# Optimization experiments

Hardware: AMD Instinct MI355X
Metric: run time of the kernel (lower is better)

The kernel has to match this reference:

```python
import jax, jax.numpy as jnp
import numpy as np

B, T, C, H = 4, 1024, 2048, 16
HD = C // H          # head dim = 128 (even, as RoPE requires)
BLOCK = 1024         # config.block_size == config.max_block_size
NEG = -1e30          # finite stand-in for -inf in the additive attention bias


def setup_inputs() -> dict:
    key = jax.random.key(0)
    k1, k2, k3, k4, k5 = jax.random.split(key, 5)
    x = jax.random.normal(k1, (B, T, C), jnp.float32)
    cumulative_scores = jax.random.uniform(k2, (B, T), jnp.float32)  # kept small: fed to exp()
    token_index = jax.random.randint(k3, (B, T), 0, BLOCK, dtype=jnp.int32)
    padding_mask = jnp.ones((B, T), jnp.int32)
    # xavier-ish scale so softmax doesn't saturate
    W_attn = jax.random.normal(k4, (C, 3 * C), jnp.float32) / np.sqrt(C)
    W_proj = jax.random.normal(k5, (C, C), jnp.float32) / np.sqrt(C)
    return dict(x=x, cumulative_scores=cumulative_scores, token_index=token_index,
                padding_mask=padding_mask, W_attn=W_attn, W_proj=W_proj)


def _rotate_half(a):
    a1, a2 = a[..., : HD // 2], a[..., HD // 2:]
    return jnp.concatenate([-a2, a1], axis=-1)


def reference(x, cumulative_scores, token_index, padding_mask, W_attn, W_proj):
    # QKV projection (bias=False per config)
    qkv = x @ W_attn                                  # (B,T,3C)
    q, k, v = jnp.split(qkv, 3, axis=2)
    heads = lambda a: a.reshape(B, T, H, HD).transpose(0, 2, 1, 3)  # (B,H,T,HD)
    q, k, v = heads(q), heads(k), heads(v)

    # input-dependent partial rotation positions (exact replica of the original
    # scatter: token_index (B,T) fancy-indexes the last axis of a (B,BLOCK)
    # buffer, so counts are summed over ALL batch rows, as in the source)
    counts = jnp.zeros((B, BLOCK), jnp.float32).at[..., token_index].add(1.0)
    t = jnp.cumsum(jnp.take_along_axis(1.0 / (counts + 1e-10), token_index, axis=-1), axis=-1)  # (B,T)

    # RoPE with per-token positions t (seq_dim=-2, offset 0 for both q and k)
    inv_freq = 1.0 / (10000.0 ** (jnp.arange(0, HD, 2, dtype=jnp.float32) / HD))
    freqs = jnp.einsum('bt,j->btj', t, inv_freq)
    emb = jnp.concatenate([freqs, freqs], axis=-1)[:, None, :, :]   # (B,1,T,HD)
    sin, cos = jnp.sin(emb), jnp.cos(emb)
    q = q * cos + _rotate_half(q) * sin
    k = k * cos + _rotate_half(k) * sin

    # 'fork' plan overrides on the last rotary channel
    q = q.at[..., -1].set(1.0)
    k = k.at[..., -1].set(jnp.broadcast_to(cumulative_scores[:, None, :], (B, H, T)))

    # V rescaled by exp(cumulative_scores)
    v = v * jnp.exp(cumulative_scores)[:, None, :, None]

    # causal + key-padding additive bias, SDPA with scale 1/sqrt(HD)
    keep = jnp.tril(jnp.ones((T, T), bool))[None, None] & padding_mask.astype(bool)[:, None, None, :]
    scores = jnp.einsum('bhqd,bhkd->bhqk', q, k) / np.sqrt(HD)
    scores = jnp.where(keep, scores, NEG)
    attn = jax.nn.softmax(scores, axis=-1)
    y = jnp.einsum('bhqk,bhkd->bhqd', attn, v)

    y = y.transpose(0, 2, 1, 3).reshape(B, T, C)
    return y @ W_proj
```

## Files before the change

kernel.cpp:

```cpp
#include <hip/hip_runtime.h>

#define BB 4
#define TT 1024
#define CCH 2048
#define HH 16
#define HDIM 128
#define NBLK 1024
#define MM (BB*TT)
#define N1 (3*CCH)
#define NQT 16

typedef _Float16 f16;
typedef _Float16 half8 __attribute__((ext_vector_type(8)));
typedef _Float16 half4 __attribute__((ext_vector_type(4)));
typedef float floatx4 __attribute__((ext_vector_type(4)));

__device__ __forceinline__ void g2lds16(const void* g, void* l) {
    __builtin_amdgcn_global_load_lds((const __attribute__((address_space(1))) void*)g,
                                     (__attribute__((address_space(3))) void*)l, 16, 0, 0);
}

__global__ void k_prep(const float* __restrict__ Wa, const float* __restrict__ Wp,
                       const float* __restrict__ x,
                       f16* __restrict__ WaT, f16* __restrict__ WpT,
                       f16* __restrict__ x16) {
    int z = blockIdx.z;
    if (z == 2) {
        int i = (blockIdx.y * 192 + blockIdx.x) * 256 + threadIdx.x + threadIdx.y * 32;
        if (i >= MM * CCH / 4) return;
        float4 v = ((const float4*)x)[i];
        union { ushort4 u; f16 h[4]; } o;
        o.h[0] = (f16)v.x; o.h[1] = (f16)v.y; o.h[2] = (f16)v.z; o.h[3] = (f16)v.w;
        ((ushort4*)x16)[i] = o.u;
        return;
    }
    const float* in = (z == 0) ? Wa : Wp;
    f16* out = (z == 0) ? WaT : WpT;
    int Cc = (z == 0) ? N1 : CCH;
    if (blockIdx.x * 32 >= Cc) return;
    __shared__ float tile[32][33];
    int c0 = blockIdx.x * 32, r0 = blockIdx.y * 32;
    int tx = threadIdx.x, ty = threadIdx.y;
#pragma unroll
    for (int k = 0; k < 4; k++) {
        int r = ty + k * 8;
        tile[r][tx] = in[(size_t)(r0 + r) * Cc + c0 + tx];
    }
    __syncthreads();
#pragma unroll
    for (int k = 0; k < 4; k++) {
        int r = ty + k * 8;
        out[(size_t)(c0 + r) * CCH + r0 + tx] = (f16)tile[tx][r];
    }
}

__global__ void k_trv(const f16* __restrict__ in, f16* __restrict__ out) {
    __shared__ f16 tile[32][34];
    int bh = blockIdx.z;
    int h0 = blockIdx.x * 32, t0 = blockIdx.y * 32;
    int tx = threadIdx.x, ty = threadIdx.y;
#pragma unroll
    for (int k = 0; k < 4; k++) {
        int t = ty + k * 8;
        tile[t][tx] = in[((size_t)bh * TT + t0 + t) * HDIM + h0 + tx];
    }
    __syncthreads();
#pragma unroll
    for (int k = 0; k < 4; k++) {
        int r = ty + k * 8;
        out[((size_t)bh * HDIM + h0 + r) * TT + t0 + tx] = tile[tx][r];
    }
}

__global__ void k_hist(const int* __restrict__ tok, int* __restrict__ cnt) {
    int i = blockIdx.x * blockDim.x + threadIdx.x;
    if (i < MM) atomicAdd(cnt + tok[i], 1);
}

__global__ __launch_bounds__(1024) void k_scan(const int* __restrict__ tok,
                                               const int* __restrict__ cnt,
                                               const int* __restrict__ pm,
                                               float* __restrict__ tpos,
                                               float* __restrict__ pb) {
    __shared__ float s[TT];
    int b = blockIdx.x, t = threadIdx.x;
    s[t] = 1.0f / ((float)cnt[tok[b * TT + t]] + 1e-10f);
    __syncthreads();
    for (int off = 1; off < TT; off <<= 1) {
        float add = (t >= off) ? s[t - off] : 0.0f;
        __syncthreads();
        s[t] += add;
        __syncthreads();
    }
    tpos[b * TT + t] = s[t];
    pb[b * TT + t] = pm[b * TT + t] ? 0.0f : -1e30f;
}

__global__ void k_rope(const float* __restrict__ tpos, float2* __restrict__ tab) {
    int i = blockIdx.x * 256 + threadIdx.x;
    int row = i >> 6, j = i & 63;
    float f = tpos[row] * expf((float)j * -0.14391156929f);
    float sn, cn; sincosf(f, &sn, &cn);
    tab[i] = make_float2(cn, sn);
}

#define RA(buf, mf, ck) (*(const half8*)((const char*)As + ((buf) << 15) + aoffb + ((mf) << 11) + (ck)))
#define RB(buf, nf, ck) (*(const half8*)((const char*)Bs + ((buf) << 15) + boffb + ((nf) << 13) + (ck)))
#define STAGE(P, L, h, t) do { \
    g2lds16((P) + ((size_t)(h) << 18) + ((t) << 6) + src0, (L) + ((h) << 13) + (w << 9)); \
    g2lds16((P) + ((size_t)(h) << 18) + ((t) << 6) + src1, (L) + ((h) << 13) + ((8 + w) << 9)); \
} while (0)
#define MFMAQ(AF, BF, M0, N0) do { \
  _Pragma("unroll") for (int m_ = 0; m_ < 4; m_++) \
  _Pragma("unroll") for (int n_ = 0; n_ < 2; n_++) \
  _Pragma("unroll") for (int k_ = 0; k_ < 2; k_++) \
    acc[(M0) + m_][(N0) + n_] = __builtin_amdgcn_mfma_f32_16x16x32_f16(AF[m_][k_], BF[n_][k_], acc[(M0) + m_][(N0) + n_], 0, 0, 0); \
} while (0)
#define BAR() __builtin_amdgcn_s_barrier()
#define WLG0() asm volatile("s_waitcnt lgkmcnt(0)" ::: "memory")

template <int MODE>
__global__ __launch_bounds__(512, 2) void k_gemm8(const f16* __restrict__ A,
                                                  const f16* __restrict__ Bt,
                                                  float* __restrict__ Cp,
                                                  const float2* __restrict__ tab,
                                                  const float* __restrict__ cs,
                                                  f16* __restrict__ qr,
                                                  f16* __restrict__ kr,
                                                  f16* __restrict__ vsc) {
    const float SCALE = 0.08838834764831845f;
    const int NBN = MODE ? 24 : 8;
    const int NWG = MODE ? 384 : 128;
    const int CPX = NWG >> 3;
    __shared__ __align__(16) f16 As[2 * 16384];
    __shared__ __align__(16) f16 Bs[2 * 16384];

    int bid = blockIdx.x;
    int s = (bid & 7) * CPX + (bid >> 3);
    int bm = s / NBN, bn = s % NBN;

    int tid = threadIdx.x;
    int w = tid >> 6, lane = tid & 63, quad = lane >> 4, l16 = lane & 15;
    int wm = w >> 2, wn = w & 3;

    const f16* Ab = A + (size_t)(bm << 8) * 2048;
    const f16* Bb = Bt + (size_t)(bn << 8) * 2048;

    int rl = lane >> 3, cl = lane & 7;
    int gl = (cl - rl) & 7;
    int src0 = (w * 8 + rl) * 2048 + gl * 8;
    int src1 = src0 + 64 * 2048;

    const int aoffb = (wm * 128 + l16) << 7;
    const int boffb = (wn * 16 + l16) << 7;
    const int ck0 = ((quad + l16) & 7) << 4;
    const int ck1 = ck0 ^ 64;

    floatx4 acc[8][4];
#pragma unroll
    for (int i = 0; i < 8; i++)
#pragma unroll
        for (int j = 0; j < 4; j++) acc[i][j] = (floatx4){0.f, 0.f, 0.f, 0.f};

    STAGE(Bb, Bs, 0, 0);
    STAGE(Ab, As, 0, 0);
    STAGE(Ab, As, 1, 0);
    STAGE(Bb, Bs, 1, 0);
    STAGE(Bb, Bs + 16384, 0, 1);
    STAGE(Ab, As + 16384, 0, 1);
    STAGE(Ab, As + 16384, 1, 1);
    asm volatile("s_waitcnt vmcnt(6)" ::: "memory");
    BAR();

#pragma unroll 1
    for (int it = 0; it < 16; ++it) {
        const int t1 = 2 * it + 1, t2 = 2 * it + 2, t3 = 2 * it + 3;
        const bool g2 = (t2 < 32), g3 = (t3 < 32);
        half8 af0[4][2], af1[4][2], bf0[2][2], bf1[2][2];
#pragma unroll
        for (int m = 0; m < 4; m++) { af0[m][0] = RA(0, m, ck0); af0[m][1] = RA(0, m, ck1); }
#pragma unroll
        for (int n = 0; n < 2; n++) { bf0[n][0] = RB(0, n, ck0); bf0[n][1] = RB(0, n, ck1); }
        STAGE(Bb, Bs + 16384, 1, t1);
        asm volatile("s_waitcnt lgkmcnt(8)" ::: "memory");
        BAR(); WLG0();
        __builtin_amdgcn_s_setprio(1); MFMAQ(af0, bf0, 0, 0); __builtin_amdgcn_s_setprio(0);
        BAR();
#pragma unroll
        for (int m = 0; m < 4; m++) { af1[m][0] = RA(0, 4 + m, ck0); af1[m][1] = RA(0, 4 + m, ck1); }
        if (g2) STAGE(Bb, Bs, 0, t2);
        BAR(); WLG0();
        __builtin_amdgcn_s_setprio(1); MFMAQ(af1, bf0, 4, 0); __builtin_amdgcn_s_setprio(0);
        BAR();
#pragma unroll
        for (int n = 0; n < 2; n++) { bf1[n][0] = RB(0, 2 + n, ck0); bf1[n][1] = RB(0, 2 + n, ck1); }
        if (g2) STAGE(Ab, As, 0, t2);
        BAR(); WLG0();
        __builtin_amdgcn_s_setprio(1); MFMAQ(af1, bf1, 4, 2); __builtin_amdgcn_s_setprio(0);
        BAR();
        if (g2) STAGE(Ab, As, 1, t2);
        BAR();
        __builtin_amdgcn_s_setprio(1); MFMAQ(af0, bf1, 0, 2); __builtin_amdgcn_s_setprio(0);
        if (it < 15) { asm volatile("s_waitcnt vmcnt(6)" ::: "memory"); }
        else         { asm volatile("s_waitcnt vmcnt(0)" ::: "memory"); }
        BAR();
#pragma unroll
        for (int m = 0; m < 4; m++) { af0[m][0] = RA(1, m, ck0); af0[m][1] = RA(1, m, ck1); }
#pragma unroll
        for (int n = 0; n < 2; n++) { bf0[n][0] = RB(1, n, ck0); bf0[n][1] = RB(1, n, ck1); }
        if (g2) STAGE(Bb, Bs, 1, t2);
        asm volatile("s_waitcnt lgkmcnt(8)" ::: "memory");
        BAR(); WLG0();
        __builtin_amdgcn_s_setprio(1); MFMAQ(af0, bf0, 0, 0); __builtin_amdgcn_s_setprio(0);
        BAR();
#pragma unroll
        for (int m = 0; m < 4; m++) { af1[m][0] = RA(1, 4 + m, ck0); af1[m][1] = RA(1, 4 + m, ck1); }
        if (g3) STAGE(Bb, Bs + 16384, 0, t3);
        BAR(); WLG0();
        __builtin_amdgcn_s_setprio(1); MFMAQ(af1, bf0, 4, 0); __builtin_amdgcn_s_setprio(0);
        BAR();
#pragma unroll
        for (int n = 0; n < 2; n++) { bf1[n][0] = RB(1, 2 + n, ck0); bf1[n][1] = RB(1, 2 + n, ck1); }
        if (g3) STAGE(Ab, As + 16384, 0, t3);
        BAR(); WLG0();
        __builtin_amdgcn_s_setprio(1); MFMAQ(af1, bf1, 4, 2); __builtin_amdgcn_s_setprio(0);
        BAR();
        if (g3) STAGE(Ab, As + 16384, 1, t3);
        BAR();
        __builtin_amdgcn_s_setprio(1); MFMAQ(af0, bf1, 0, 2); __builtin_amdgcn_s_setprio(0);
        if (it < 15) { asm volatile("s_waitcnt vmcnt(6)" ::: "memory"); }
        else         { asm volatile("s_waitcnt vmcnt(0)" ::: "memory"); }
        BAR();
    }

    if (MODE == 0) {
#pragma unroll
        for (int mf = 0; mf < 8; mf++)
#pragma unroll
            for (int nf = 0; nf < 4; nf++) {
                int col = (bn << 8) + wn * 16 + nf * 64 + l16;
#pragma unroll
                for (int r = 0; r < 4; r++) {
                    int row = (bm << 8) + wm * 128 + mf * 16 + (quad << 2) + r;
                    Cp[(size_t)row * CCH + col] = acc[mf][nf][r];
                }
            }
    } else {
        int type = bn >> 3;
        int h0 = (bn * 2) & 15;
        int d1 = wn * 16 + l16;
        if (type < 2) {
            f16* outp = (type == 0) ? qr : kr;
#pragma unroll
            for (int mf = 0; mf < 8; mf++)
#pragma unroll
                for (int r = 0; r < 4; r++) {
                    int row = (bm << 8) + wm * 128 + mf * 16 + (quad << 2) + r;
                    float2 tc = tab[row * 64 + d1];
#pragma unroll
                    for (int p = 0; p < 2; p++) {
                        float a1 = acc[mf][2 * p][r], a2 = acc[mf][2 * p + 1][r];
                        float o1 = a1 * tc.x - a2 * tc.y;
                        float o2 = a2 * tc.x + a1 * tc.y;
                        if (type == 0) {
                            if (d1 == 63) o2 = 1.0f;
                            o1 *= SCALE; o2 *= SCALE;
                        } else {
                            if (d1 == 63) o2 = cs[row];
                        }
                        size_t ob = ((size_t)((row >> 10) * HH + h0 + p) * TT + (row & 1023)) * HDIM + d1;
                        outp[ob] = (f16)o1;
                        outp[ob + 64] = (f16)o2;
                    }
                }
        } else {
#pragma unroll
            for (int mf = 0; mf < 8; mf++)
#pragma unroll
                for (int r = 0; r < 4; r++) {
                    int row = (bm << 8) + wm * 128 + mf * 16 + (quad << 2) + r;
                    float ve = __expf(cs[row]);
#pragma unroll
                    for (int nf = 0; nf < 4; nf++) {
                        int d = ((nf & 1) << 6) + d1;
                        size_t ob = ((size_t)((row >> 10) * HH + h0 + (nf >> 1)) * TT + (row & 1023)) * HDIM + d;
                        vsc[ob] = (f16)(acc[mf][nf][r] * ve);
                    }
                }
        }
    }
}

__global__ __launch_bounds__(256) void k_attn(const f16* __restrict__ qr,
                                              const f16* __restrict__ kr,
                                              const f16* __restrict__ vt,
                                              const float* __restrict__ pb,
                                              f16* __restrict__ y) {
    __shared__ __align__(16) f16 Ks[64 * 136];
    __shared__ __align__(16) f16 Vs[128 * 72];
    __shared__ float pbs[64];
    int p = blockIdx.x & (NQT / 2 - 1);
    int bh = blockIdx.x >> 3;
    int b = bh >> 4, h = bh & 15;
    int tid = threadIdx.x;
    int w = tid >> 6, lane = tid & 63, quad = lane >> 4, l16 = lane & 15;
#pragma unroll
    for (int pass = 0; pass < 2; pass++) {
        int qt = pass ? (NQT - 1 - p) : p;
        int q0 = qt << 6;
        int qg = q0 + w * 16 + l16;
        const f16* Qp = qr + ((size_t)bh * TT + qg) * HDIM;
        half8 qf[4];
#pragma unroll
        for (int kc = 0; kc < 4; kc++) qf[kc] = *(const half8*)&Qp[kc * 32 + (quad << 3)];
        floatx4 O[8];
#pragma unroll
        for (int i = 0; i < 8; i++) O[i] = (floatx4){0.f, 0.f, 0.f, 0.f};
        float mx = -1e30f, ls = 0.f;
        for (int kt = 0; kt <= qt; kt++) {
            __syncthreads();
            const f16* Kb = kr + ((size_t)bh * TT + (kt << 6)) * HDIM;
            const f16* Vb = vt + (size_t)bh * HDIM * TT + (kt << 6);
#pragma unroll
            for (int i = 0; i < 4; i++) {
                int seg = tid + (i << 8);
                int krow = seg >> 4, kcol = (seg & 15) << 3;
                *(uint4*)&Ks[krow * 136 + kcol] = *(const uint4*)&Kb[(size_t)krow * HDIM + kcol];
                int vrow = seg >> 3, vcol = (seg & 7) << 3;
                *(uint4*)&Vs[vrow * 72 + vcol] = *(const uint4*)&Vb[(size_t)vrow * TT + vcol];
            }
            if (tid < 64) pbs[tid] = pb[b * TT + (kt << 6) + tid];
            __syncthreads();
            floatx4 Sv[4];
#pragma unroll
            for (int mc = 0; mc < 4; mc++) Sv[mc] = (floatx4){0.f, 0.f, 0.f, 0.f};
#pragma unroll
            for (int kc = 0; kc < 4; kc++)
#pragma unroll
                for (int mc = 0; mc < 4; mc++) {
                    half8 kf = *(const half8*)&Ks[(mc * 16 + l16) * 136 + kc * 32 + (quad << 3)];
                    Sv[mc] = __builtin_amdgcn_mfma_f32_16x16x32_f16(kf, qf[kc], Sv[mc], 0, 0, 0);
                }
            float pv[4][4];
            float mnew = mx;
#pragma unroll
            for (int mc = 0; mc < 4; mc++) {
                float4 pbv = *(const float4*)&pbs[mc * 16 + (quad << 2)];
#pragma unroll
                for (int i = 0; i < 4; i++) {
                    int kv = (kt << 6) + mc * 16 + (quad << 2) + i;
                    float s = (kv <= qg) ? Sv[mc][i] + ((const float*)&pbv)[i] : -1e30f;
                    pv[mc][i] = s;
                    mnew = fmaxf(mnew, s);
                }
            }
            mnew = fmaxf(mnew, __shfl_xor(mnew, 16));
            mnew = fmaxf(mnew, __shfl_xor(mnew, 32));
            float al = __expf(mx - mnew);
            mx = mnew;
            float psum = 0.f;
#pragma unroll
            for (int mc = 0; mc < 4; mc++)
#pragma unroll
                for (int i = 0; i < 4; i++) {
                    float e = __expf(pv[mc][i] - mnew);
                    pv[mc][i] = e;
                    psum += e;
                }
            psum += __shfl_xor(psum, 16);
            psum += __shfl_xor(psum, 32);
            ls = ls * al + psum;
#pragma unroll
            for (int hm = 0; hm < 8; hm++)
#pragma unroll
                for (int i = 0; i < 4; i++) O[hm][i] *= al;
            half4 pf[4];
#pragma unroll
            for (int mc = 0; mc < 4; mc++) {
                pf[mc][0] = (f16)pv[mc][0]; pf[mc][1] = (f16)pv[mc][1];
                pf[mc][2] = (f16)pv[mc][2]; pf[mc][3] = (f16)pv[mc][3];
            }
#pragma unroll
            for (int mc = 0; mc < 4; mc++)
#pragma unroll
                for (int hm = 0; hm < 8; hm++) {
                    half4 vf = *(const half4*)&Vs[(hm * 16 + l16) * 72 + mc * 16 + (quad << 2)];
                    O[hm] = __builtin_amdgcn_mfma_f32_16x16x16f16(vf, pf[mc], O[hm], 0, 0, 0);
                }
        }
        float inv = 1.0f / ls;
#pragma unroll
        for (int hm = 0; hm < 8; hm++) {
            half4 ov;
#pragma unroll
            for (int i = 0; i < 4; i++) ov[i] = (f16)(O[hm][i] * inv);
            *(half4*)&y[((size_t)b * TT + qg) * CCH + h * HDIM + hm * 16 + (quad << 2)] = ov;
        }
        __syncthreads();
    }
}

extern "C" void kernel_launch(void* const* d_in, const int* in_sizes, int n_in,
                              void* d_out, int out_size, void* d_ws, size_t ws_size,
                              hipStream_t stream) {
    const float* x   = (const float*)d_in[0];
    const float* cs  = (const float*)d_in[1];
    const int*   tok = (const int*)d_in[2];
    const int*   pm  = (const int*)d_in[3];
    const float* Wa  = (const float*)d_in[4];
    const float* Wp  = (const float*)d_in[5];
    float* out = (float*)d_out;
    char* ws = (char*)d_ws;

    f16* x16 = (f16*)(ws + 0);
    f16* WaT = (f16*)(ws + 16777216);
    f16* vt  = (f16*)(ws + 41943040);
    f16* WpT = (f16*)(ws + 58720256);
    float2* tab = (float2*)(ws + 67108864);
    f16* qr  = (f16*)(ws + 92274688);
    f16* kr  = (f16*)(ws + 109051904);
    f16* vsc = (f16*)(ws + 125829120);
    int*   cnt  = (int*)(ws + 142606336);
    float* tpos = (float*)(ws + 142610432);
    float* pb   = (float*)(ws + 142626816);
    f16* y   = x16;

    hipMemsetAsync(cnt, 0, NBLK * sizeof(int), stream);
    k_hist<<<MM / 256, 256, 0, stream>>>(tok, cnt);
    k_scan<<<BB, TT, 0, stream>>>(tok, cnt, pm, tpos, pb);
    k_rope<<<MM * 64 / 256, 256, 0, stream>>>(tpos, tab);
    k_prep<<<dim3(N1 / 32, CCH / 32, 3), dim3(32, 8), 0, stream>>>(Wa, Wp, x, WaT, WpT, x16);
    k_gemm8<1><<<384, 512, 0, stream>>>(x16, WaT, nullptr, tab, cs, qr, kr, vsc);
    k_trv<<<dim3(4, 32, BB * HH), dim3(32, 8), 0, stream>>>(vsc, vt);
    k_attn<<<BB * HH * (NQT / 2), 256, 0, stream>>>(qr, kr, vt, pb, y);
    k_gemm8<0><<<128, 512, 0, stream>>>(y, WpT, out, nullptr, nullptr, nullptr, nullptr, nullptr);
}
```

Baseline: 421.1 us.

## Shrink GEMM N-tile to 128 and simplify to two-phase LDS pipeline

The shared GEMM kernel drops from 256x256 tiles to 256x128 tiles. That doubles the workgroup count for the QKV projection (768) and the output projection (256), giving better occupancy across the 256 CUs, and halves the B-side LDS. The complex interleaved schedule with partial vmcnt waits is replaced by a simpler ping-pong: full-K fragment reads alternate between register sets, and every half-step waits with vmcnt(0). The epilogues are rewritten so each workgroup writes one head's RoPE'd Q/K or scaled V. The trade-offs are lower arithmetic intensity per tile and a possible loss of load/compute overlap from the stricter waits.

```diff
diff --git a/kernel.cpp b/kernel.cpp
--- a/kernel.cpp
+++ b/kernel.cpp
@@ -104,20 +104,20 @@
     tab[i] = make_float2(cn, sn);
 }
 
-#define RA(buf, mf, ck) (*(const half8*)((const char*)As + ((buf) << 15) + aoffb + ((mf) << 11) + (ck)))
-#define RB(buf, nf, ck) (*(const half8*)((const char*)Bs + ((buf) << 15) + boffb + ((nf) << 13) + (ck)))
-#define STAGE(P, L, h, t) do { \
-    g2lds16((P) + ((size_t)(h) << 18) + ((t) << 6) + src0, (L) + ((h) << 13) + (w << 9)); \
-    g2lds16((P) + ((size_t)(h) << 18) + ((t) << 6) + src1, (L) + ((h) << 13) + ((8 + w) << 9)); \
-} while (0)
-#define MFMAQ(AF, BF, M0, N0) do { \
-  _Pragma("unroll") for (int m_ = 0; m_ < 4; m_++) \
-  _Pragma("unroll") for (int n_ = 0; n_ < 2; n_++) \
-  _Pragma("unroll") for (int k_ = 0; k_ < 2; k_++) \
-    acc[(M0) + m_][(N0) + n_] = __builtin_amdgcn_mfma_f32_16x16x32_f16(AF[m_][k_], BF[n_][k_], acc[(M0) + m_][(N0) + n_], 0, 0, 0); \
-} while (0)
 #define BAR() __builtin_amdgcn_s_barrier()
-#define WLG0() asm volatile("s_waitcnt lgkmcnt(0)" ::: "memory")
+#define RDA(S, buf, ck) do { _Pragma("unroll") for (int m_ = 0; m_ < 8; m_++) \
+    S[m_] = *(const half8*)((const char*)As + ((buf) << 15) + aoffb + (m_ << 11) + (ck)); } while (0)
+#define RDB(S, buf, ck) do { _Pragma("unroll") for (int n_ = 0; n_ < 2; n_++) \
+    S[n_] = *(const half8*)((const char*)Bs + ((buf) << 14) + boffb + (n_ << 13) + (ck)); } while (0)
+#define STAGEA(t, lofs) do { _Pragma("unroll") for (int k_ = 0; k_ < 4; k_++) \
+    g2lds16(Ab + (size_t)(k_ * 64) * 2048 + ((t) << 6) + srcr, \
+            (char*)As + (lofs) + (w * 8 + k_ * 64) * 128); } while (0)
+#define STAGEB(t, lofs) do { _Pragma("unroll") for (int k_ = 0; k_ < 2; k_++) \
+    g2lds16(Bb + (size_t)(k_ * 64) * 2048 + ((t) << 6) + srcr, \
+            (char*)Bs + (lofs) + (w * 8 + k_ * 64) * 128); } while (0)
+#define MF16(SA, SB) do { _Pragma("unroll") for (int m_ = 0; m_ < 8; m_++) \
+    _Pragma("unroll") for (int n_ = 0; n_ < 2; n_++) \
+    acc[m_][n_] = __builtin_amdgcn_mfma_f32_16x16x32_f16(SA[m_], SB[n_], acc[m_][n_], 0, 0, 0); } while (0)
 
 template <int MODE>
 __global__ __launch_bounds__(512, 2) void k_gemm8(const f16* __restrict__ A,
@@ -129,11 +129,11 @@
                                                   f16* __restrict__ kr,
                                                   f16* __restrict__ vsc) {
     const float SCALE = 0.08838834764831845f;
-    const int NBN = MODE ? 24 : 8;
-    const int NWG = MODE ? 384 : 128;
+    const int NBN = MODE ? 48 : 16;
+    const int NWG = MODE ? 768 : 256;
     const int CPX = NWG >> 3;
     __shared__ __align__(16) f16 As[2 * 16384];
-    __shared__ __align__(16) f16 Bs[2 * 16384];
+    __shared__ __align__(16) f16 Bs[2 * 8192];
 
     int bid = blockIdx.x;
     int s = (bid & 7) * CPX + (bid >> 3);
@@ -144,101 +144,59 @@
     int wm = w >> 2, wn = w & 3;
 
     const f16* Ab = A + (size_t)(bm << 8) * 2048;
-    const f16* Bb = Bt + (size_t)(bn << 8) * 2048;
+    const f16* Bb = Bt + (size_t)(bn << 7) * 2048;
 
     int rl = lane >> 3, cl = lane & 7;
     int gl = (cl - rl) & 7;
-    int src0 = (w * 8 + rl) * 2048 + gl * 8;
-    int src1 = src0 + 64 * 2048;
+    int srcr = (w * 8 + rl) * 2048 + gl * 8;
 
     const int aoffb = (wm * 128 + l16) << 7;
     const int boffb = (wn * 16 + l16) << 7;
     const int ck0 = ((quad + l16) & 7) << 4;
     const int ck1 = ck0 ^ 64;
 
-    floatx4 acc[8][4];
+    floatx4 acc[8][2];
 #pragma unroll
     for (int i = 0; i < 8; i++)
 #pragma unroll
-        for (int j = 0; j < 4; j++) acc[i][j] = (floatx4){0.f, 0.f, 0.f, 0.f};
-
-    STAGE(Bb, Bs, 0, 0);
-    STAGE(Ab, As, 0, 0);
-    STAGE(Ab, As, 1, 0);
-    STAGE(Bb, Bs, 1, 0);
-    STAGE(Bb, Bs + 16384, 0, 1);
-    STAGE(Ab, As + 16384, 0, 1);
-    STAGE(Ab, As + 16384, 1, 1);
+        for (int j = 0; j < 2; j++) acc[i][j] = (floatx4){0.f, 0.f, 0.f, 0.f};
+
+    half8 S0a[8], S1a[8];
+    half8 S0b[2], S1b[2];
+
+    STAGEA(0, 0);      STAGEB(0, 0);
+    STAGEA(1, 32768);  STAGEB(1, 16384);
     asm volatile("s_waitcnt vmcnt(6)" ::: "memory");
     BAR();
+    RDA(S0a, 0, ck0); RDB(S0b, 0, ck0);
 
 #pragma unroll 1
-    for (int it = 0; it < 16; ++it) {
-        const int t1 = 2 * it + 1, t2 = 2 * it + 2, t3 = 2 * it + 3;
-        const bool g2 = (t2 < 32), g3 = (t3 < 32);
-        half8 af0[4][2], af1[4][2], bf0[2][2], bf1[2][2];
-#pragma unroll
-        for (int m = 0; m < 4; m++) { af0[m][0] = RA(0, m, ck0); af0[m][1] = RA(0, m, ck1); }
-#pragma unroll
-        for (int n = 0; n < 2; n++) { bf0[n][0] = RB(0, n, ck0); bf0[n][1] = RB(0, n, ck1); }
-        STAGE(Bb, Bs + 16384, 1, t1);
-        asm volatile("s_waitcnt lgkmcnt(8)" ::: "memory");
-        BAR(); WLG0();
-        __builtin_amdgcn_s_setprio(1); MFMAQ(af0, bf0, 0, 0); __builtin_amdgcn_s_setprio(0);
+    for (int i = 0; i < 16; ++i) {
+        const int t2 = 2 * i + 2, t3 = 2 * i + 3;
+        RDA(S1a, 0, ck1); RDB(S1b, 0, ck1);
+        __builtin_amdgcn_s_setprio(1); MF16(S0a, S0b); __builtin_amdgcn_s_setprio(0);
+        asm volatile("s_waitcnt vmcnt(0)" ::: "memory");
         BAR();
-#pragma unroll
-        for (int m = 0; m < 4; m++) { af1[m][0] = RA(0, 4 + m, ck0); af1[m][1] = RA(0, 4 + m, ck1); }
-        if (g2) STAGE(Bb, Bs, 0, t2);
-        BAR(); WLG0();
-        __builtin_amdgcn_s_setprio(1); MFMAQ(af1, bf0, 4, 0); __builtin_amdgcn_s_setprio(0);
+        RDA(S0a, 1, ck0); RDB(S0b, 1, ck0);
+        if (t2 < 32) { STAGEA(t2, 0); STAGEB(t2, 0); }
+        __builtin_amdgcn_s_setprio(1); MF16(S1a, S1b); __builtin_amdgcn_s_setprio(0);
         BAR();
-#pragma unroll
-        for (int n = 0; n < 2; n++) { bf1[n][0] = RB(0, 2 + n, ck0); bf1[n][1] = RB(0, 2 + n, ck1); }
-        if (g2) STAGE(Ab, As, 0, t2);
-        BAR(); WLG0();
-        __builtin_amdgcn_s_setprio(1); MFMAQ(af1, bf1, 4, 2); __builtin_amdgcn_s_setprio(0);
+        RDA(S1a, 1, ck1); RDB(S1b, 1, ck1);
+        __builtin_amdgcn_s_setprio(1); MF16(S0a, S0b); __builtin_amdgcn_s_setprio(0);
+        asm volatile("s_waitcnt vmcnt(0)" ::: "memory");
         BAR();
-        if (g2) STAGE(Ab, As, 1, t2);
+        RDA(S0a, 0, ck0); RDB(S0b, 0, ck0);
+        if (t3 < 32) { STAGEA(t3, 32768); STAGEB(t3, 16384); }
+        __builtin_amdgcn_s_setprio(1); MF16(S1a, S1b); __builtin_amdgcn_s_setprio(0);
         BAR();
-        __builtin_amdgcn_s_setprio(1); MFMAQ(af0, bf1, 0, 2); __builtin_amdgcn_s_setprio(0);
-        if (it < 15) { asm volatile("s_waitcnt vmcnt(6)" ::: "memory"); }
-        else         { asm volatile("s_waitcnt vmcnt(0)" ::: "memory"); }
-        BAR();
-#pragma unroll
-        for (int m = 0; m < 4; m++) { af0[m][0] = RA(1, m, ck0); af0[m][1] = RA(1, m, ck1); }
-#pragma unroll
-        for (int n = 0; n < 2; n++) { bf0[n][0] = RB(1, n, ck0); bf0[n][1] = RB(1, n, ck1); }
-        if (g2) STAGE(Bb, Bs, 1, t2);
-        asm volatile("s_waitcnt lgkmcnt(8)" ::: "memory");
-        BAR(); WLG0();
-        __builtin_amdgcn_s_setprio(1); MFMAQ(af0, bf0, 0, 0); __builtin_amdgcn_s_setprio(0);
-        BAR();
-#pragma unroll
-        for (int m = 0; m < 4; m++) { af1[m][0] = RA(1, 4 + m, ck0); af1[m][1] = RA(1, 4 + m, ck1); }
-        if (g3) STAGE(Bb, Bs + 16384, 0, t3);
-        BAR(); WLG0();
-        __builtin_amdgcn_s_setprio(1); MFMAQ(af1, bf0, 4, 0); __builtin_amdgcn_s_setprio(0);
-        BAR();
-#pragma unroll
-        for (int n = 0; n < 2; n++) { bf1[n][0] = RB(1, 2 + n, ck0); bf1[n][1] = RB(1, 2 + n, ck1); }
-        if (g3) STAGE(Ab, As + 16384, 0, t3);
-        BAR(); WLG0();
-        __builtin_amdgcn_s_setprio(1); MFMAQ(af1, bf1, 4, 2); __builtin_amdgcn_s_setprio(0);
-        BAR();
-        if (g3) STAGE(Ab, As + 16384, 1, t3);
-        BAR();
-        __builtin_amdgcn_s_setprio(1); MFMAQ(af0, bf1, 0, 2); __builtin_amdgcn_s_setprio(0);
-        if (it < 15) { asm volatile("s_waitcnt vmcnt(6)" ::: "memory"); }
-        else         { asm volatile("s_waitcnt vmcnt(0)" ::: "memory"); }
-        BAR();
     }
 
     if (MODE == 0) {
 #pragma unroll
         for (int mf = 0; mf < 8; mf++)
 #pragma unroll
-            for (int nf = 0; nf < 4; nf++) {
-                int col = (bn << 8) + wn * 16 + nf * 64 + l16;
+            for (int nf = 0; nf < 2; nf++) {
+                int col = (bn << 7) + wn * 16 + nf * 64 + l16;
 #pragma unroll
                 for (int r = 0; r < 4; r++) {
                     int row = (bm << 8) + wm * 128 + mf * 16 + (quad << 2) + r;
@@ -246,8 +204,8 @@
                 }
             }
     } else {
-        int type = bn >> 3;
-        int h0 = (bn * 2) & 15;
+        int type = bn >> 4;
+        int h = bn & 15;
         int d1 = wn * 16 + l16;
         if (type < 2) {
             f16* outp = (type == 0) ? qr : kr;
@@ -257,21 +215,18 @@
                 for (int r = 0; r < 4; r++) {
                     int row = (bm << 8) + wm * 128 + mf * 16 + (quad << 2) + r;
                     float2 tc = tab[row * 64 + d1];
-#pragma unroll
-                    for (int p = 0; p < 2; p++) {
-                        float a1 = acc[mf][2 * p][r], a2 = acc[mf][2 * p + 1][r];
-                        float o1 = a1 * tc.x - a2 * tc.y;
-                        float o2 = a2 * tc.x + a1 * tc.y;
-                        if (type == 0) {
-                            if (d1 == 63) o2 = 1.0f;
-                            o1 *= SCALE; o2 *= SCALE;
-                        } else {
-                            if (d1 == 63) o2 = cs[row];
-                        }
-                        size_t ob = ((size_t)((row >> 10) * HH + h0 + p) * TT + (row & 1023)) * HDIM + d1;
-                        outp[ob] = (f16)o1;
-                        outp[ob + 64] = (f16)o2;
+                    float a1 = acc[mf][0][r], a2 = acc[mf][1][r];
+                    float o1 = a1 * tc.x - a2 * tc.y;
+                    float o2 = a2 * tc.x + a1 * tc.y;
+                    if (type == 0) {
+                        if (d1 == 63) o2 = 1.0f;
+                        o1 *= SCALE; o2 *= SCALE;
+                    } else {
+                        if (d1 == 63) o2 = cs[row];
                     }
+                    size_t ob = ((size_t)((row >> 10) * HH + h) * TT + (row & 1023)) * HDIM + d1;
+                    outp[ob] = (f16)o1;
+                    outp[ob + 64] = (f16)o2;
                 }
         } else {
 #pragma unroll
@@ -280,12 +235,9 @@
                 for (int r = 0; r < 4; r++) {
                     int row = (bm << 8) + wm * 128 + mf * 16 + (quad << 2) + r;
                     float ve = __expf(cs[row]);
-#pragma unroll
-                    for (int nf = 0; nf < 4; nf++) {
-                        int d = ((nf & 1) << 6) + d1;
-                        size_t ob = ((size_t)((row >> 10) * HH + h0 + (nf >> 1)) * TT + (row & 1023)) * HDIM + d;
-                        vsc[ob] = (f16)(acc[mf][nf][r] * ve);
-                    }
+                    size_t ob = ((size_t)((row >> 10) * HH + h) * TT + (row & 1023)) * HDIM + d1;
+                    vsc[ob]      = (f16)(acc[mf][0][r] * ve);
+                    vsc[ob + 64] = (f16)(acc[mf][1][r] * ve);
                 }
         }
     }
@@ -430,8 +382,8 @@
     k_scan<<<BB, TT, 0, stream>>>(tok, cnt, pm, tpos, pb);
     k_rope<<<MM * 64 / 256, 256, 0, stream>>>(tpos, tab);
     k_prep<<<dim3(N1 / 32, CCH / 32, 3), dim3(32, 8), 0, stream>>>(Wa, Wp, x, WaT, WpT, x16);
-    k_gemm8<1><<<384, 512, 0, stream>>>(x16, WaT, nullptr, tab, cs, qr, kr, vsc);
+    k_gemm8<1><<<768, 512, 0, stream>>>(x16, WaT, nullptr, tab, cs, qr, kr, vsc);
     k_trv<<<dim3(4, 32, BB * HH), dim3(32, 8), 0, stream>>>(vsc, vt);
     k_attn<<<BB * HH * (NQT / 2), 256, 0, stream>>>(qr, kr, vt, pb, y);
-    k_gemm8<0><<<128, 512, 0, stream>>>(y, WpT, out, nullptr, nullptr, nullptr, nullptr, nullptr);
-}
+    k_gemm8<0><<<256, 512, 0, stream>>>(y, WpT, out, nullptr, nullptr, nullptr, nullptr, nullptr);
+}
```

Measured after the change: 385.0 us. 8.6% less time.
